# Optimization experiments

Hardware: AMD Instinct MI355X
Metric: run time of the kernel (lower is better)

Reference implementation:

```python
import jax, jax.numpy as jnp
import numpy as np

N = 10000      # nodes
E = 160000     # edges
F_IN = 84
H = 256
P = 4          # powers [0,1,2,3]
L = 3          # mixhop layers


def setup_inputs() -> dict:
    key = jax.random.key(0)
    ks = jax.random.split(key, 10)
    s = 0.05
    inp = {}
    inp["x"] = jax.random.normal(ks[0], (N, F_IN), jnp.float32)
    inp["edge_index"] = jax.random.randint(ks[1], (2, E), 0, N, dtype=jnp.int32)
    inp["w_in"] = jax.random.normal(ks[2], (F_IN, H), jnp.float32) * s
    inp["b_in"] = jnp.zeros((H,), jnp.float32)
    inp["mh_w0"] = jax.random.normal(ks[3], (P, H, H), jnp.float32) * s
    inp["mh_b0"] = jnp.zeros((P, H), jnp.float32)
    inp["mh_w12"] = jax.random.normal(ks[4], (2, P, P * H, H), jnp.float32) * s
    inp["mh_b12"] = jnp.zeros((2, P, H), jnp.float32)
    inp["ln_g"] = jnp.ones((L, P * H), jnp.float32)
    inp["ln_b"] = jnp.zeros((L, P * H), jnp.float32)
    inp["w1"] = jax.random.normal(ks[5], (P * H, H), jnp.float32) * s
    inp["b1"] = jnp.zeros((H,), jnp.float32)
    inp["w2"] = jax.random.normal(ks[6], (H, H // 2), jnp.float32) * s
    inp["b2"] = jnp.zeros((H // 2,), jnp.float32)
    inp["w3"] = jax.random.normal(ks[7], (H // 2, 1), jnp.float32) * s
    inp["b3"] = jnp.zeros((1,), jnp.float32)
    return inp


def _gcn_norm(edge_index, n):
    # D^{-1/2} (A + I) D^{-1/2}, PyG gcn_norm with add_self_loops=True
    loop = jnp.arange(n, dtype=edge_index.dtype)
    src = jnp.concatenate([edge_index[0], loop])
    dst = jnp.concatenate([edge_index[1], loop])
    deg = jax.ops.segment_sum(jnp.ones(src.shape[0], jnp.float32), dst, num_segments=n)
    dinv = jnp.where(deg > 0, deg ** -0.5, 0.0)
    return src, dst, dinv[src] * dinv[dst]


def _propagate(h, src, dst, w, n):
    # out[i] = sum_{(j->i)} w_e * h[j]
    return jax.ops.segment_sum(h[src] * w[:, None], dst, num_segments=n)


def _mixhop(h, src, dst, w, n, W, B):
    outs = [h @ W[0] + B[0]]  # power 0
    for p in range(1, W.shape[0]):
        h = _propagate(h, src, dst, w, n)
        outs.append(h @ W[p] + B[p])
    return jnp.concatenate(outs, axis=-1)  # [n, P*H]


def _layernorm(x, g, b, eps=1e-5):
    mu = x.mean(-1, keepdims=True)
    var = x.var(-1, keepdims=True)
    return (x - mu) * jax.lax.rsqrt(var + eps) * g + b


def reference(x, edge_index, w_in, b_in, mh_w0, mh_b0, mh_w12, mh_b12,
              ln_g, ln_b, w1, b1, w2, b2, w3, b3):
    gelu = lambda t: jax.nn.gelu(t, approximate=False)  # torch default (erf)
    n = x.shape[0]
    src, dst, w = _gcn_norm(edge_index, n)
    h = gelu(x @ w_in + b_in)
    for i in range(L):
        W, B = (mh_w0, mh_b0) if i == 0 else (mh_w12[i - 1], mh_b12[i - 1])
        h = _mixhop(h, src, dst, w, n, W, B)
        h = gelu(_layernorm(h, ln_g[i], ln_b[i]))
        # dropout inactive at inference
    h = gelu(h @ w1 + b1)
    h = gelu(h @ w2 + b2)
    out = h @ w3 + b3
    return out.squeeze(-1)  # [N]
```

## Files before the change

### kernel.cpp

```cpp
#include <hip/hip_runtime.h>

typedef unsigned short u16;
typedef unsigned int u32;
typedef __bf16 bf16x8 __attribute__((ext_vector_type(8)));
typedef float f32x4 __attribute__((ext_vector_type(4)));

#define NN 10000
#define EE 160000
#define MPAD 10112

__device__ inline float b2f(u16 u) { return __uint_as_float(((u32)u) << 16); }
__device__ inline u16 f2b(float f) {
    u32 u = __float_as_uint(f);
    return (u16)((u + 0x7fffu + ((u >> 16) & 1u)) >> 16);
}
__device__ inline float gelu_f(float x) {
    return 0.5f * x * (1.0f + erff(x * 0.70710678118654752f));
}
__device__ inline void load_lds16(const u16* g, u16* l) {
    __builtin_amdgcn_global_load_lds((const __attribute__((address_space(1))) u32*)g,
                                     (__attribute__((address_space(3))) u32*)l, 16, 0, 0);
}

__global__ __launch_bounds__(256) void k_count(const int* __restrict__ dst, int* __restrict__ cnt) {
    int e = blockIdx.x * 256 + threadIdx.x;
    if (e < EE) atomicAdd(&cnt[dst[e]], 1);
}

__global__ __launch_bounds__(256) void k_scan(const int* __restrict__ cnt, int* __restrict__ rowptr,
                                              int* __restrict__ cursor, float* __restrict__ dinv) {
    __shared__ int part[256];
    const int t = threadIdx.x;
    const int CH = 40;
    int base = t * CH;
    int ssum = 0;
    for (int k = 0; k < CH; k++) { int i = base + k; if (i < NN) ssum += cnt[i]; }
    part[t] = ssum;
    __syncthreads();
    for (int off = 1; off < 256; off <<= 1) {
        int v = (t >= off) ? part[t - off] : 0;
        __syncthreads();
        part[t] += v;
        __syncthreads();
    }
    int run = part[t] - ssum;
    for (int k = 0; k < CH; k++) {
        int i = base + k;
        if (i < NN) {
            rowptr[i] = run; cursor[i] = run;
            int c = cnt[i];
            dinv[i] = rsqrtf((float)(c + 1));
            run += c;
        }
    }
    if (t == 255) rowptr[NN] = run;
}

__global__ __launch_bounds__(256) void k_fill(const int* __restrict__ src, const int* __restrict__ dst,
                                              int* __restrict__ cursor, int* __restrict__ cols,
                                              float* __restrict__ vals, const float* __restrict__ dinv) {
    int e = blockIdx.x * 256 + threadIdx.x;
    if (e < EE) {
        int s = src[e], d = dst[e];
        int pos = atomicAdd(&cursor[d], 1);
        cols[pos] = s;
        vals[pos] = dinv[s] * dinv[d];
    }
}

__global__ __launch_bounds__(256) void k_padx(const float* __restrict__ x, u16* __restrict__ xp) {
    int idx = blockIdx.x * 256 + threadIdx.x;
    if (idx >= MPAD * 96) return;
    int r = idx / 96, c = idx - r * 96;
    u16 v = 0;
    if (r < NN && c < 84) v = f2b(x[(size_t)r * 84 + c]);
    xp[idx] = v;
}

struct TT { const float* src; u16* dst; int K, Nc, Kp; };
__global__ __launch_bounds__(256) void k_transT(TT t0, TT t1, TT t2, TT t3, TT t4) {
    int b = blockIdx.x; TT T;
    if (b < 8)        { T = t0; }
    else if (b < 72)  { T = t1; b -= 8; }
    else if (b < 584) { T = t2; b -= 72; }
    else if (b < 648) { T = t3; b -= 584; }
    else              { T = t4; b -= 648; }
    int tk = (T.K + 63) >> 6, tn = T.Nc >> 6;
    int bb  = b / (tk * tn);
    int rem = b - bb * (tk * tn);
    int k0 = (rem / tn) * 64, n0 = (rem % tn) * 64;
    __shared__ u16 tile[64][65];
    const float* src = T.src + (size_t)bb * T.K * T.Nc;
    u16* dst = T.dst + (size_t)bb * T.Nc * T.Kp;
    int c = threadIdx.x & 63, r0 = threadIdx.x >> 6;
#pragma unroll
    for (int i = 0; i < 16; i++) {
        int r = r0 + i * 4;
        int k = k0 + r;
        u16 v = 0;
        if (k < T.K) v = f2b(src[(size_t)k * T.Nc + n0 + c]);
        tile[r][c] = v;
    }
    __syncthreads();
    int rr = threadIdx.x & 63, cc0 = threadIdx.x >> 6;
#pragma unroll
    for (int i = 0; i < 16; i++) {
        int cc = cc0 + i * 4;
        int k = k0 + rr;
        if (k < T.Kp) dst[(size_t)(n0 + cc) * T.Kp + k] = tile[rr][cc];
    }
}

struct CvtSrcs { const float *b_in, *mh_b0, *mh_b12, *ln_g, *ln_b, *b1, *b2, *w3, *b3; };
__global__ __launch_bounds__(256) void k_cvt_all(CvtSrcs S, u16* __restrict__ dst) {
    int i = blockIdx.x * 256 + threadIdx.x;
    const float* s; int base;
    if (i < 256)       { s = S.b_in;   base = 0; }
    else if (i < 1280) { s = S.mh_b0;  base = 256; }
    else if (i < 3328) { s = S.mh_b12; base = 1280; }
    else if (i < 6400) { s = S.ln_g;   base = 3328; }
    else if (i < 9472) { s = S.ln_b;   base = 6400; }
    else if (i < 9728) { s = S.b1;     base = 9472; }
    else if (i < 9856) { s = S.b2;     base = 9728; }
    else if (i < 9984) { s = S.w3;     base = 9856; }
    else if (i < 9985) { s = S.b3;     base = 9984; }
    else return;
    dst[i] = f2b(s[i - base]);
}

template<int TM, int TN, int ACT, int EPI, int BATCH>
__global__ __launch_bounds__(256) void k_gemm(const u16* __restrict__ A0, const u16* __restrict__ A1,
                                              const u16* __restrict__ A2, const u16* __restrict__ A3,
                                              const u16* __restrict__ Bt, const u16* __restrict__ bias,
                                              u16* __restrict__ C, u16* __restrict__ Z,
                                              int K, int ldc, int col0, int NB_M, int NB_N) {
    constexpr int AM = TM / 32, AN = TN / 32;
    constexpr int CA = TM / 16, CB = TN / 16;
    constexpr int NCH = (CA + CB) / 4;
    __shared__ __align__(16) u16 As[2][TM * 32];
    __shared__ __align__(16) u16 Bs[2][TN * 32];
    int id = blockIdx.x;
    int g8 = id & 7, sIdx = id >> 3;
    int nb = sIdx % NB_N, jb = sIdx / NB_N;
    int mb = g8 + 8 * jb;
    if (mb >= NB_M) return;
    const u16* A = A0;
    if (BATCH) {
        int z = blockIdx.y;
        if (z == 1) A = A1; else if (z == 2) A = A2; else if (z == 3) A = A3;
        Bt   += (size_t)z * 256 * K;
        bias += z * 256;
        col0 += z * 256;
    }
    const int t = threadIdx.x;
    const int wv = t >> 6, lane = t & 63;
    const int wm = wv >> 1, wn = wv & 1;
    const int quad = lane >> 4, l16 = lane & 15;
    const int tileM = mb * TM, tileN = nb * TN;

    f32x4 acc[AM][AN] = {};

    const int rch = lane >> 2, c8 = (lane & 3) * 8;
    const u16* gsrc[NCH];
    u16* l0[NCH]; u16* l1[NCH];
#pragma unroll
    for (int i = 0; i < NCH; i++) {
        int c = wv + 4 * i;
        if (c < CA) {
            gsrc[i] = A + (size_t)(tileM + c * 16 + rch) * K + c8;
            l0[i] = &As[0][c * 512 + lane * 8];
            l1[i] = &As[1][c * 512 + lane * 8];
        } else {
            int cc = c - CA;
            gsrc[i] = Bt + (size_t)(tileN + cc * 16 + rch) * K + c8;
            l0[i] = &Bs[0][cc * 512 + lane * 8];
            l1[i] = &Bs[1][cc * 512 + lane * 8];
        }
    }

#pragma unroll
    for (int i = 0; i < NCH; i++) load_lds16(gsrc[i], l0[i]);

    int kb = 0;
    for (int k0 = 0; k0 < K; k0 += 32, kb ^= 1) {
        __syncthreads();
        if (k0 + 32 < K) {
#pragma unroll
            for (int i = 0; i < NCH; i++)
                load_lds16(gsrc[i] + k0 + 32, kb ? l0[i] : l1[i]);
        }
        const u16* Ab = As[kb];
        const u16* Bb = Bs[kb];
        bf16x8 af[AM], bfr[AN];
#pragma unroll
        for (int tm = 0; tm < AM; tm++)
            af[tm] = *(const bf16x8*)&Ab[(wm * (TM / 2) + tm * 16 + l16) * 32 + quad * 8];
#pragma unroll
        for (int tn = 0; tn < AN; tn++)
            bfr[tn] = *(const bf16x8*)&Bb[(wn * (TN / 2) + tn * 16 + l16) * 32 + quad * 8];
#pragma unroll
        for (int tm = 0; tm < AM; tm++)
#pragma unroll
            for (int tn = 0; tn < AN; tn++)
                acc[tm][tn] = __builtin_amdgcn_mfma_f32_16x16x32_bf16(af[tm], bfr[tn], acc[tm][tn], 0, 0, 0);
    }

#pragma unroll
    for (int tm = 0; tm < AM; tm++)
#pragma unroll
        for (int tn = 0; tn < AN; tn++)
#pragma unroll
            for (int r = 0; r < 4; r++) {
                int row = tileM + wm * (TM / 2) + tm * 16 + quad * 4 + r;
                int col = tileN + wn * (TN / 2) + tn * 16 + l16;
                float v = acc[tm][tn][r];
                if (EPI == 2) {
                    if (col < 256) C[(size_t)row * 1024 + col] = f2b(v + b2f(bias[col]));
                    else           Z[(size_t)row * 768 + (col - 256)] = f2b(v);
                } else {
                    v += b2f(bias[col]);
                    if (ACT) v = gelu_f(v);
                    C[(size_t)row * ldc + col0 + col] = f2b(v);
                }
            }
}

template<int CAT0>
__global__ __launch_bounds__(256) void k_propw(const u16* __restrict__ hin, int W, int G,
                                               const int* __restrict__ rowptr, const int* __restrict__ cols,
                                               const float* __restrict__ vals, const float* __restrict__ dinv,
                                               u16* __restrict__ concat, const u16* __restrict__ bias,
                                               int col0, u16* __restrict__ out2) {
    int unit = blockIdx.x * 4 + (threadIdx.x >> 6);
    if (unit >= NN * G) return;
    int node = unit / G, g = unit - node * G;
    int lane = threadIdx.x & 63;
    int half = lane >> 5, fl = lane & 31;
    const u16* base = hin + g * 256 + fl * 8;
    float a0 = 0, a1 = 0, a2 = 0, a3 = 0, a4 = 0, a5 = 0, a6 = 0, a7 = 0;
    if (half == 1) {
        float di = dinv[node], sw = di * di;
        bf16x8 sv = *(const bf16x8*)(base + (size_t)node * W);
        a0 = sw * (float)sv[0]; a1 = sw * (float)sv[1]; a2 = sw * (float)sv[2]; a3 = sw * (float)sv[3];
        a4 = sw * (float)sv[4]; a5 = sw * (float)sv[5]; a6 = sw * (float)sv[6]; a7 = sw * (float)sv[7];
    }
    int s = rowptr[node], e = rowptr[node + 1];
    int q = s + half;
    for (; q + 6 < e; q += 8) {
        int j0 = cols[q], j1 = cols[q + 2], j2 = cols[q + 4], j3 = cols[q + 6];
        float w0 = vals[q], w1 = vals[q + 2], w2 = vals[q + 4], w3 = vals[q + 6];
        bf16x8 v0 = *(const bf16x8*)(base + (size_t)j0 * W);
        bf16x8 v1 = *(const bf16x8*)(base + (size_t)j1 * W);
        bf16x8 v2 = *(const bf16x8*)(base + (size_t)j2 * W);
        bf16x8 v3 = *(const bf16x8*)(base + (size_t)j3 * W);
        a0 += w0 * (float)v0[0] + w1 * (float)v1[0] + w2 * (float)v2[0] + w3 * (float)v3[0];
        a1 += w0 * (float)v0[1] + w1 * (float)v1[1] + w2 * (float)v2[1] + w3 * (float)v3[1];
        a2 += w0 * (float)v0[2] + w1 * (float)v1[2] + w2 * (float)v2[2] + w3 * (float)v3[2];
        a3 += w0 * (float)v0[3] + w1 * (float)v1[3] + w2 * (float)v2[3] + w3 * (float)v3[3];
        a4 += w0 * (float)v0[4] + w1 * (float)v1[4] + w2 * (float)v2[4] + w3 * (float)v3[4];
        a5 += w0 * (float)v0[5] + w1 * (float)v1[5] + w2 * (float)v2[5] + w3 * (float)v3[5];
        a6 += w0 * (float)v0[6] + w1 * (float)v1[6] + w2 * (float)v2[6] + w3 * (float)v3[6];
        a7 += w0 * (float)v0[7] + w1 * (float)v1[7] + w2 * (float)v2[7] + w3 * (float)v3[7];
    }
    for (; q + 2 < e; q += 4) {
        int j0 = cols[q], j1 = cols[q + 2];
        float w0 = vals[q], w1 = vals[q + 2];
        bf16x8 v0 = *(const bf16x8*)(base + (size_t)j0 * W);
        bf16x8 v1 = *(const bf16x8*)(base + (size_t)j1 * W);
        a0 += w0 * (float)v0[0] + w1 * (float)v1[0];
        a1 += w0 * (float)v0[1] + w1 * (float)v1[1];
        a2 += w0 * (float)v0[2] + w1 * (float)v1[2];
        a3 += w0 * (float)v0[3] + w1 * (float)v1[3];
        a4 += w0 * (float)v0[4] + w1 * (float)v1[4];
        a5 += w0 * (float)v0[5] + w1 * (float)v1[5];
        a6 += w0 * (float)v0[6] + w1 * (float)v1[6];
        a7 += w0 * (float)v0[7] + w1 * (float)v1[7];
    }
    if (q < e) {
        int j = cols[q];
        float w = vals[q];
        bf16x8 v = *(const bf16x8*)(base + (size_t)j * W);
        a0 += w * (float)v[0]; a1 += w * (float)v[1]; a2 += w * (float)v[2]; a3 += w * (float)v[3];
        a4 += w * (float)v[4]; a5 += w * (float)v[5]; a6 += w * (float)v[6]; a7 += w * (float)v[7];
    }
    a0 += __shfl_down(a0, 32); a1 += __shfl_down(a1, 32);
    a2 += __shfl_down(a2, 32); a3 += __shfl_down(a3, 32);
    a4 += __shfl_down(a4, 32); a5 += __shfl_down(a5, 32);
    a6 += __shfl_down(a6, 32); a7 += __shfl_down(a7, 32);
    if (half == 0) {
        int f = fl * 8;
        union { u16 u[8]; uint4 v; } pk;
        if (CAT0 && g == 0) {
            pk.u[0] = f2b(a0 + b2f(bias[f + 0])); pk.u[1] = f2b(a1 + b2f(bias[f + 1]));
            pk.u[2] = f2b(a2 + b2f(bias[f + 2])); pk.u[3] = f2b(a3 + b2f(bias[f + 3]));
            pk.u[4] = f2b(a4 + b2f(bias[f + 4])); pk.u[5] = f2b(a5 + b2f(bias[f + 5]));
            pk.u[6] = f2b(a6 + b2f(bias[f + 6])); pk.u[7] = f2b(a7 + b2f(bias[f + 7]));
            *(uint4*)(concat + (size_t)node * 1024 + col0 + f) = pk.v;
        } else {
            int W2 = W - CAT0 * 256;
            pk.u[0] = f2b(a0); pk.u[1] = f2b(a1); pk.u[2] = f2b(a2); pk.u[3] = f2b(a3);
            pk.u[4] = f2b(a4); pk.u[5] = f2b(a5); pk.u[6] = f2b(a6); pk.u[7] = f2b(a7);
            *(uint4*)(out2 + (size_t)node * W2 + (g - CAT0) * 256 + f) = pk.v;
        }
    }
}

__global__ __launch_bounds__(256) void k_ln_gelu(const u16* __restrict__ X, const u16* __restrict__ g,
                                                 const u16* __restrict__ b, u16* __restrict__ out) {
    __shared__ float red[256];
    const int row = blockIdx.x, t = threadIdx.x;
    ushort4 xv = *(const ushort4*)(X + (size_t)row * 1024 + t * 4);
    float x0 = b2f(xv.x), x1 = b2f(xv.y), x2 = b2f(xv.z), x3 = b2f(xv.w);
    red[t] = x0 + x1 + x2 + x3;
    __syncthreads();
    for (int off = 128; off; off >>= 1) {
        if (t < off) red[t] += red[t + off];
        __syncthreads();
    }
    float mu = red[0] * (1.f / 1024.f);
    __syncthreads();
    float d0 = x0 - mu, d1 = x1 - mu, d2 = x2 - mu, d3 = x3 - mu;
    red[t] = d0 * d0 + d1 * d1 + d2 * d2 + d3 * d3;
    __syncthreads();
    for (int off = 128; off; off >>= 1) {
        if (t < off) red[t] += red[t + off];
        __syncthreads();
    }
    float rs = rsqrtf(red[0] * (1.f / 1024.f) + 1e-5f);
    int c = t * 4;
    ushort4 gv = *(const ushort4*)(g + c);
    ushort4 bv = *(const ushort4*)(b + c);
    ushort4 o;
    o.x = f2b(gelu_f(d0 * rs * b2f(gv.x) + b2f(bv.x)));
    o.y = f2b(gelu_f(d1 * rs * b2f(gv.y) + b2f(bv.y)));
    o.z = f2b(gelu_f(d2 * rs * b2f(gv.z) + b2f(bv.z)));
    o.w = f2b(gelu_f(d3 * rs * b2f(gv.w) + b2f(bv.w)));
    *(ushort4*)(out + (size_t)row * 1024 + c) = o;
}

__global__ __launch_bounds__(256) void k_final(const u16* __restrict__ h, const u16* __restrict__ w3,
                                               const u16* __restrict__ b3, float* __restrict__ out) {
    int gw = (blockIdx.x * 256 + threadIdx.x) >> 6;
    int lane = threadIdx.x & 63;
    if (gw >= NN) return;
    u32 hv = *(const u32*)(h + (size_t)gw * 128 + lane * 2);
    u32 wv = *(const u32*)(w3 + lane * 2);
    float s = b2f((u16)(hv & 0xffff)) * b2f((u16)(wv & 0xffff)) +
              b2f((u16)(hv >> 16)) * b2f((u16)(wv >> 16));
    for (int off = 32; off; off >>= 1) s += __shfl_down(s, off);
    if (lane == 0) out[gw] = s + b2f(b3[0]);
}

extern "C" void kernel_launch(void* const* d_in, const int* in_sizes, int n_in,
                              void* d_out, int out_size, void* d_ws, size_t ws_size,
                              hipStream_t stream) {
    (void)in_sizes; (void)n_in; (void)out_size; (void)ws_size;
    const float* x  = (const float*)d_in[0];
    const int*   ei = (const int*)d_in[1];
    float* out = (float*)d_out;

    char* p = (char*)d_ws;
    auto alloc = [&](size_t bytes) { char* q = p; p += (bytes + 255) & ~(size_t)255; return q; };
    int*   cnt    = (int*)alloc(NN * 4);
    int*   rowptr = (int*)alloc((NN + 1) * 4);
    int*   cursor = (int*)alloc(NN * 4);
    float* dinv   = (float*)alloc(NN * 4);
    int*   cols   = (int*)alloc(EE * 4);
    float* vals   = (float*)alloc(EE * 4);
    u16*   xp     = (u16*)alloc((size_t)MPAD * 96 * 2);
    u16*   wbuf   = (u16*)alloc((size_t)2678784 * 2);
    u16*   smallC = (u16*)alloc(10240 * 2);
    u16*   S1     = (u16*)alloc((size_t)MPAD * 256 * 2);
    u16*   S2     = (u16*)alloc((size_t)MPAD * 256 * 2);
    u16*   S3     = (u16*)alloc((size_t)MPAD * 256 * 2);
    u16*   S4     = (u16*)alloc((size_t)MPAD * 256 * 2);
    u16*   Zb     = (u16*)alloc((size_t)MPAD * 768 * 2);
    u16*   Y2     = (u16*)alloc((size_t)MPAD * 512 * 2);
    u16*   Y3     = (u16*)alloc((size_t)MPAD * 256 * 2);
    u16*   bufA   = (u16*)alloc((size_t)MPAD * 1024 * 2);
    u16*   concat = (u16*)alloc((size_t)MPAD * 1024 * 2);

    u16* winT  = wbuf;
    u16* w0T   = wbuf + 24576;
    u16* w12T  = wbuf + 286720;
    u16* w1T   = wbuf + 2383872;
    u16* w2T   = wbuf + 2646016;
    u16* binC  = smallC;
    u16* mb0C  = smallC + 256;
    u16* mb12C = smallC + 1280;
    u16* lngC  = smallC + 3328;
    u16* lnbC  = smallC + 6400;
    u16* b1C   = smallC + 9472;
    u16* b2C   = smallC + 9728;
    u16* w3C   = smallC + 9856;
    u16* b3C   = smallC + 9984;

    const int* srcA = ei;
    const int* dstA = ei + EE;

    hipMemsetAsync(cnt, 0, NN * 4, stream);

    k_padx<<<(MPAD * 96 + 255) / 256, 256, 0, stream>>>(x, xp);
    TT t0{(const float*)d_in[2],  winT, 84,   256, 96};
    TT t1{(const float*)d_in[4],  w0T,  256,  256, 256};
    TT t2{(const float*)d_in[6],  w12T, 1024, 256, 1024};
    TT t3{(const float*)d_in[10], w1T,  1024, 256, 1024};
    TT t4{(const float*)d_in[12], w2T,  256,  128, 256};
    k_transT<<<656, 256, 0, stream>>>(t0, t1, t2, t3, t4);
    CvtSrcs CS{(const float*)d_in[3], (const float*)d_in[5], (const float*)d_in[7],
               (const float*)d_in[8], (const float*)d_in[9], (const float*)d_in[11],
               (const float*)d_in[13], (const float*)d_in[14], (const float*)d_in[15]};
    k_cvt_all<<<40, 256, 0, stream>>>(CS, smallC);

    k_count<<<(EE + 255) / 256, 256, 0, stream>>>(dstA, cnt);
    k_scan<<<1, 256, 0, stream>>>(cnt, rowptr, cursor, dinv);
    k_fill<<<(EE + 255) / 256, 256, 0, stream>>>(srcA, dstA, cursor, cols, vals, dinv);

    auto gx = [](int nbm, int nbn) { return 8 * ((nbm + 7) / 8) * nbn; };

    k_gemm<128, 64, 1, 0, 0><<<gx(79, 4), 256, 0, stream>>>(xp, xp, xp, xp, winT, binC, S1, nullptr, 96, 256, 0, 79, 4);

    k_propw<0><<<2500, 256, 0, stream>>>(S1, 256, 1, rowptr, cols, vals, dinv, nullptr, nullptr, 0, S2);
    k_propw<0><<<2500, 256, 0, stream>>>(S2, 256, 1, rowptr, cols, vals, dinv, nullptr, nullptr, 0, S3);
    k_propw<0><<<2500, 256, 0, stream>>>(S3, 256, 1, rowptr, cols, vals, dinv, nullptr, nullptr, 0, S4);
    k_gemm<128, 64, 0, 0, 1><<<dim3(gx(79, 4), 4), 256, 0, stream>>>(S1, S2, S3, S4, w0T, mb0C, concat, nullptr, 256, 1024, 0, 79, 4);
    k_ln_gelu<<<NN, 256, 0, stream>>>(concat, lngC, lnbC, bufA);

    for (int L = 0; L < 2; L++) {
        const u16* WT = w12T + (size_t)L * 1024 * 1024;
        const u16* BB = mb12C + L * 1024;
        k_gemm<128, 64, 0, 2, 0><<<gx(79, 16), 256, 0, stream>>>(bufA, bufA, bufA, bufA, WT, BB, concat, Zb, 1024, 0, 0, 79, 16);
        k_propw<1><<<7500, 256, 0, stream>>>(Zb, 768, 3, rowptr, cols, vals, dinv, concat, BB + 256, 256, Y2);
        k_propw<1><<<5000, 256, 0, stream>>>(Y2, 512, 2, rowptr, cols, vals, dinv, concat, BB + 512, 512, Y3);
        k_propw<1><<<2500, 256, 0, stream>>>(Y3, 256, 1, rowptr, cols, vals, dinv, concat, BB + 768, 768, Y3);
        k_ln_gelu<<<NN, 256, 0, stream>>>(concat, lngC + (L + 1) * 1024, lnbC + (L + 1) * 1024, bufA);
    }

    k_gemm<64, 64, 1, 0, 0><<<gx(158, 4), 256, 0, stream>>>(bufA, bufA, bufA, bufA, w1T, b1C, S1, nullptr, 1024, 256, 0, 158, 4);
    k_gemm<64, 64, 1, 0, 0><<<gx(158, 2), 256, 0, stream>>>(S1, S1, S1, S1, w2T, b2C, S2, nullptr, 256, 128, 0, 158, 2);
    k_final<<<2500, 256, 0, stream>>>(S2, w3C, b3C, out);
}
```

Baseline: 505.2 us.

## Process two K-slices per GEMM barrier and reorder propagation work by group

Result: faster. 479.9 us (-5.0%).

```diff
diff --git a/kernel.cpp b/kernel.cpp
--- a/kernel.cpp
+++ b/kernel.cpp
@@ -70,8 +70,8 @@
 
 __global__ __launch_bounds__(256) void k_padx(const float* __restrict__ x, u16* __restrict__ xp) {
     int idx = blockIdx.x * 256 + threadIdx.x;
-    if (idx >= MPAD * 96) return;
-    int r = idx / 96, c = idx - r * 96;
+    if (idx >= MPAD * 128) return;
+    int r = idx >> 7, c = idx & 127;
     u16 v = 0;
     if (r < NN && c < 84) v = f2b(x[(size_t)r * 84 + c]);
     xp[idx] = v;
@@ -85,7 +85,7 @@
     else if (b < 584) { T = t2; b -= 72; }
     else if (b < 648) { T = t3; b -= 584; }
     else              { T = t4; b -= 648; }
-    int tk = (T.K + 63) >> 6, tn = T.Nc >> 6;
+    int tk = (T.Kp + 63) >> 6, tn = T.Nc >> 6;
     int bb  = b / (tk * tn);
     int rem = b - bb * (tk * tn);
     int k0 = (rem / tn) * 64, n0 = (rem % tn) * 64;
@@ -137,8 +137,8 @@
     constexpr int AM = TM / 32, AN = TN / 32;
     constexpr int CA = TM / 16, CB = TN / 16;
     constexpr int NCH = (CA + CB) / 4;
-    __shared__ __align__(16) u16 As[2][TM * 32];
-    __shared__ __align__(16) u16 Bs[2][TN * 32];
+    constexpr int SLOT = (TM + TN) * 32;
+    __shared__ __align__(16) u16 Sh[4][SLOT];
     int id = blockIdx.x;
     int g8 = id & 7, sIdx = id >> 3;
     int nb = sIdx % NB_N, jb = sIdx / NB_N;
@@ -162,47 +162,53 @@
 
     const int rch = lane >> 2, c8 = (lane & 3) * 8;
     const u16* gsrc[NCH];
-    u16* l0[NCH]; u16* l1[NCH];
+    int lofs[NCH];
 #pragma unroll
     for (int i = 0; i < NCH; i++) {
         int c = wv + 4 * i;
         if (c < CA) {
             gsrc[i] = A + (size_t)(tileM + c * 16 + rch) * K + c8;
-            l0[i] = &As[0][c * 512 + lane * 8];
-            l1[i] = &As[1][c * 512 + lane * 8];
+            lofs[i] = c * 512 + lane * 8;
         } else {
             int cc = c - CA;
             gsrc[i] = Bt + (size_t)(tileN + cc * 16 + rch) * K + c8;
-            l0[i] = &Bs[0][cc * 512 + lane * 8];
-            l1[i] = &Bs[1][cc * 512 + lane * 8];
+            lofs[i] = TM * 32 + cc * 512 + lane * 8;
         }
     }
 
 #pragma unroll
-    for (int i = 0; i < NCH; i++) load_lds16(gsrc[i], l0[i]);
-
-    int kb = 0;
-    for (int k0 = 0; k0 < K; k0 += 32, kb ^= 1) {
+    for (int i = 0; i < NCH; i++) load_lds16(gsrc[i], &Sh[0][lofs[i]]);
+#pragma unroll
+    for (int i = 0; i < NCH; i++) load_lds16(gsrc[i] + 32, &Sh[1][lofs[i]]);
+
+    const int npair = K >> 6;
+    for (int p = 0; p < npair; p++) {
         __syncthreads();
-        if (k0 + 32 < K) {
-#pragma unroll
-            for (int i = 0; i < NCH; i++)
-                load_lds16(gsrc[i] + k0 + 32, kb ? l0[i] : l1[i]);
+        int cur = (p & 1) << 1;
+        int nxt = cur ^ 2;
+        int kc = p << 6;
+        if (kc + 64 < K) {
+#pragma unroll
+            for (int i = 0; i < NCH; i++) load_lds16(gsrc[i] + kc + 64, &Sh[nxt][lofs[i]]);
+#pragma unroll
+            for (int i = 0; i < NCH; i++) load_lds16(gsrc[i] + kc + 96, &Sh[nxt + 1][lofs[i]]);
         }
-        const u16* Ab = As[kb];
-        const u16* Bb = Bs[kb];
-        bf16x8 af[AM], bfr[AN];
-#pragma unroll
-        for (int tm = 0; tm < AM; tm++)
-            af[tm] = *(const bf16x8*)&Ab[(wm * (TM / 2) + tm * 16 + l16) * 32 + quad * 8];
-#pragma unroll
-        for (int tn = 0; tn < AN; tn++)
-            bfr[tn] = *(const bf16x8*)&Bb[(wn * (TN / 2) + tn * 16 + l16) * 32 + quad * 8];
-#pragma unroll
-        for (int tm = 0; tm < AM; tm++)
+#pragma unroll
+        for (int h = 0; h < 2; h++) {
+            const u16* S = Sh[cur + h];
+            bf16x8 af[AM], bfr[AN];
+#pragma unroll
+            for (int tm = 0; tm < AM; tm++)
+                af[tm] = *(const bf16x8*)&S[(wm * (TM / 2) + tm * 16 + l16) * 32 + quad * 8];
 #pragma unroll
             for (int tn = 0; tn < AN; tn++)
-                acc[tm][tn] = __builtin_amdgcn_mfma_f32_16x16x32_bf16(af[tm], bfr[tn], acc[tm][tn], 0, 0, 0);
+                bfr[tn] = *(const bf16x8*)&S[TM * 32 + (wn * (TN / 2) + tn * 16 + l16) * 32 + quad * 8];
+#pragma unroll
+            for (int tm = 0; tm < AM; tm++)
+#pragma unroll
+                for (int tn = 0; tn < AN; tn++)
+                    acc[tm][tn] = __builtin_amdgcn_mfma_f32_16x16x32_bf16(af[tm], bfr[tn], acc[tm][tn], 0, 0, 0);
+        }
     }
 
 #pragma unroll
@@ -233,7 +239,7 @@
                                                int col0, u16* __restrict__ out2) {
     int unit = blockIdx.x * 4 + (threadIdx.x >> 6);
     if (unit >= NN * G) return;
-    int node = unit / G, g = unit - node * G;
+    int g = unit / NN, node = unit - g * NN;
     int lane = threadIdx.x & 63;
     int half = lane >> 5, fl = lane & 31;
     const u16* base = hin + g * 256 + fl * 8;
@@ -367,8 +373,8 @@
     float* dinv   = (float*)alloc(NN * 4);
     int*   cols   = (int*)alloc(EE * 4);
     float* vals   = (float*)alloc(EE * 4);
-    u16*   xp     = (u16*)alloc((size_t)MPAD * 96 * 2);
-    u16*   wbuf   = (u16*)alloc((size_t)2678784 * 2);
+    u16*   xp     = (u16*)alloc((size_t)MPAD * 128 * 2);
+    u16*   wbuf   = (u16*)alloc((size_t)2686976 * 2);
     u16*   smallC = (u16*)alloc(10240 * 2);
     u16*   S1     = (u16*)alloc((size_t)MPAD * 256 * 2);
     u16*   S2     = (u16*)alloc((size_t)MPAD * 256 * 2);
@@ -381,10 +387,10 @@
     u16*   concat = (u16*)alloc((size_t)MPAD * 1024 * 2);
 
     u16* winT  = wbuf;
-    u16* w0T   = wbuf + 24576;
-    u16* w12T  = wbuf + 286720;
-    u16* w1T   = wbuf + 2383872;
-    u16* w2T   = wbuf + 2646016;
+    u16* w0T   = wbuf + 32768;
+    u16* w12T  = wbuf + 294912;
+    u16* w1T   = wbuf + 2392064;
+    u16* w2T   = wbuf + 2654208;
     u16* binC  = smallC;
     u16* mb0C  = smallC + 256;
     u16* mb12C = smallC + 1280;
@@ -400,8 +406,8 @@
 
     hipMemsetAsync(cnt, 0, NN * 4, stream);
 
-    k_padx<<<(MPAD * 96 + 255) / 256, 256, 0, stream>>>(x, xp);
-    TT t0{(const float*)d_in[2],  winT, 84,   256, 96};
+    k_padx<<<(MPAD * 128 + 255) / 256, 256, 0, stream>>>(x, xp);
+    TT t0{(const float*)d_in[2],  winT, 84,   256, 128};
     TT t1{(const float*)d_in[4],  w0T,  256,  256, 256};
     TT t2{(const float*)d_in[6],  w12T, 1024, 256, 1024};
     TT t3{(const float*)d_in[10], w1T,  1024, 256, 1024};
@@ -418,7 +424,7 @@
 
     auto gx = [](int nbm, int nbn) { return 8 * ((nbm + 7) / 8) * nbn; };
 
-    k_gemm<128, 64, 1, 0, 0><<<gx(79, 4), 256, 0, stream>>>(xp, xp, xp, xp, winT, binC, S1, nullptr, 96, 256, 0, 79, 4);
+    k_gemm<128, 64, 1, 0, 0><<<gx(79, 4), 256, 0, stream>>>(xp, xp, xp, xp, winT, binC, S1, nullptr, 128, 256, 0, 79, 4);
 
     k_propw<0><<<2500, 256, 0, stream>>>(S1, 256, 1, rowptr, cols, vals, dinv, nullptr, nullptr, 0, S2);
     k_propw<0><<<2500, 256, 0, stream>>>(S2, 256, 1, rowptr, cols, vals, dinv, nullptr, nullptr, 0, S3);
```
